# Performance work log

Hardware: AMD Instinct MI355X
Metric: run time of the kernel (lower is better)

## Reference

```python
import jax, jax.numpy as jnp
import numpy as np

EMBED_DIM = 1024
NUM_HEADS = 16
HEAD_DIM = EMBED_DIM // NUM_HEADS
BATCH = 2
SEQ = 2048


def setup_inputs() -> dict:
    key = jax.random.key(0)
    ks = jax.random.split(key, 9)
    scale = 1.0 / np.sqrt(EMBED_DIM)
    return {
        "inputs": jax.random.normal(ks[0], (BATCH, SEQ, EMBED_DIM), jnp.float32),
        "Wq": jax.random.normal(ks[1], (EMBED_DIM, EMBED_DIM), jnp.float32) * scale,
        "bq": jnp.zeros((EMBED_DIM,), jnp.float32),
        "Wk": jax.random.normal(ks[2], (EMBED_DIM, EMBED_DIM), jnp.float32) * scale,
        "bk": jnp.zeros((EMBED_DIM,), jnp.float32),
        "Wv": jax.random.normal(ks[3], (EMBED_DIM, EMBED_DIM), jnp.float32) * scale,
        "bv": jnp.zeros((EMBED_DIM,), jnp.float32),
        "Wo": jax.random.normal(ks[4], (EMBED_DIM, EMBED_DIM), jnp.float32) * scale,
        "bo": jnp.zeros((EMBED_DIM,), jnp.float32),
    }


def reference(inputs, Wq, bq, Wk, bk, Wv, bv, Wo, bo):
    B, S, D = inputs.shape
    H, Dh = NUM_HEADS, HEAD_DIM

    def split_heads(x):  # [B,S,D] -> [B,H,S,Dh]
        return x.reshape(B, S, H, Dh).transpose(0, 2, 1, 3)

    Q = split_heads(inputs @ Wq + bq)
    K = split_heads(inputs @ Wk + bk)
    V = split_heads(inputs @ Wv + bv)

    # naive full-score attention, faithful to the original
    scores = jnp.einsum("bhqd,bhkd->bhqk", Q, K) / jnp.sqrt(jnp.float32(Dh))
    weights = jax.nn.softmax(scores, axis=-1)
    out = jnp.einsum("bhqk,bhkd->bhqd", weights, V)

    concat = out.transpose(0, 2, 1, 3).reshape(B, S, D)
    return concat @ Wo + bo
```

## Files before the change

kernel.cpp:

```cpp
#include <hip/hip_runtime.h>

#define EMBED 1024
#define NHEAD 16
#define HDIM  64
#define BATCH 2
#define SEQ   2048
#define MTOK  (BATCH * SEQ)

typedef __bf16 bf16x8 __attribute__((ext_vector_type(8)));
typedef __bf16 bf16x4 __attribute__((ext_vector_type(4)));
typedef float  f32x4  __attribute__((ext_vector_type(4)));

__device__ __forceinline__ unsigned short f2bf(float f) {
  unsigned int u = __float_as_uint(f);
  u += 0x7fffu + ((u >> 16) & 1u);
  return (unsigned short)(u >> 16);
}
__device__ __forceinline__ __bf16 f2bf16(float f) {
  unsigned short s = f2bf(f);
  return *reinterpret_cast<__bf16*>(&s);
}

__device__ __forceinline__ void gload_lds16(const unsigned short* g, unsigned short* l) {
  __builtin_amdgcn_global_load_lds((__attribute__((address_space(1))) void*)g,
                                   (__attribute__((address_space(3))) void*)l, 16, 0, 0);
}

__global__ void cast_bf16_k(const float* __restrict__ src,
                            unsigned short* __restrict__ dst, int n4) {
  int i = blockIdx.x * blockDim.x + threadIdx.x;
  if (i < n4) {
    float4 f = reinterpret_cast<const float4*>(src)[i];
    ushort4 u;
    u.x = f2bf(f.x); u.y = f2bf(f.y); u.z = f2bf(f.z); u.w = f2bf(f.w);
    reinterpret_cast<ushort4*>(dst)[i] = u;
  }
}

__global__ __launch_bounds__(256)
void transpose_cast4_k(const float* __restrict__ s0, const float* __restrict__ s1,
                       const float* __restrict__ s2, const float* __restrict__ s3,
                       unsigned short* __restrict__ d0, unsigned short* __restrict__ d1,
                       unsigned short* __restrict__ d2, unsigned short* __restrict__ d3) {
  const float* s; unsigned short* d;
  switch (blockIdx.z) {
    case 0: s = s0; d = d0; break;
    case 1: s = s1; d = d1; break;
    case 2: s = s2; d = d2; break;
    default: s = s3; d = d3; break;
  }
  __shared__ unsigned short T[64][65];
  const int k0 = blockIdx.x * 64, n0 = blockIdx.y * 64;
  for (int i = threadIdx.x; i < 4096; i += 256) {
    int r = i >> 6, c = i & 63;
    T[c][r] = f2bf(s[(size_t)(k0 + r) * EMBED + n0 + c]);
  }
  __syncthreads();
  for (int i = threadIdx.x; i < 4096; i += 256) {
    int r = i >> 6, c = i & 63;
    d[(size_t)(n0 + r) * EMBED + k0 + c] = T[r][c];
  }
}

template<int MODE, int BM>
__global__ __launch_bounds__(256, 2)
void gemm_k(const unsigned short* __restrict__ A,
            const unsigned short* __restrict__ Bt,
            const float* __restrict__ b0, const float* __restrict__ b1,
            const float* __restrict__ b2,
            unsigned short* __restrict__ oQ, unsigned short* __restrict__ oK,
            unsigned short* __restrict__ oV, float* __restrict__ oF) {
  constexpr int MI = BM / 32;
  __shared__ unsigned short As[BM][64];
  __shared__ unsigned short Bs[128][64];
  const int tid = threadIdx.x, lane = tid & 63, wave = tid >> 6;
  const int lr = lane & 15, quad = lane >> 4;
  const int wm = (wave >> 1) * (BM / 2), wn = (wave & 1) * 64;
  const int row0 = blockIdx.x * BM, col0 = blockIdx.y * 128;
  const int srow = lane >> 3, sc = lane & 7;
  const int sw0 = (quad ^ (lr & 7)) * 8;
  const int sw1 = ((quad ^ 4) ^ (lr & 7)) * 8;

  const f32x4 fz = {0.f, 0.f, 0.f, 0.f};
  f32x4 acc[MI][4];
#pragma unroll
  for (int i = 0; i < MI; ++i)
#pragma unroll
    for (int j = 0; j < 4; ++j) acc[i][j] = fz;

  for (int k0 = 0; k0 < EMBED; k0 += 64) {
#pragma unroll
    for (int g = 0; g < BM / 32; ++g) {
      int rbase = wave * (BM / 4) + g * 8;
      int row = rbase + srow;
      gload_lds16(&A[(size_t)(row0 + row) * EMBED + k0 + ((sc ^ (row & 7)) * 8)],
                  &As[rbase][0]);
    }
#pragma unroll
    for (int g = 0; g < 4; ++g) {
      int rbase = wave * 32 + g * 8;
      int row = rbase + srow;
      gload_lds16(&Bt[(size_t)(col0 + row) * EMBED + k0 + ((sc ^ (row & 7)) * 8)],
                  &Bs[rbase][0]);
    }
    __syncthreads();
#pragma unroll
    for (int kk = 0; kk < 64; kk += 32) {
      const int so = (kk == 0) ? sw0 : sw1;
      bf16x8 af[MI], bv[4];
#pragma unroll
      for (int i = 0; i < MI; ++i)
        af[i] = *reinterpret_cast<const bf16x8*>(&As[wm + i * 16 + lr][so]);
#pragma unroll
      for (int j = 0; j < 4; ++j)
        bv[j] = *reinterpret_cast<const bf16x8*>(&Bs[wn + j * 16 + lr][so]);
#pragma unroll
      for (int i = 0; i < MI; ++i)
#pragma unroll
        for (int j = 0; j < 4; ++j)
          acc[i][j] = __builtin_amdgcn_mfma_f32_16x16x32_bf16(af[i], bv[j],
                                                              acc[i][j], 0, 0, 0);
    }
    __syncthreads();
  }

#pragma unroll
  for (int i = 0; i < MI; ++i) {
#pragma unroll
    for (int j = 0; j < 4; ++j) {
      const int col = col0 + wn + j * 16 + lr;
      if (MODE == 1) {
        const float bb = b0[col];
#pragma unroll
        for (int r = 0; r < 4; ++r) {
          const int row = row0 + wm + i * 16 + quad * 4 + r;
          oF[((size_t)row << 10) + col] = acc[i][j][r] + bb;
        }
      } else {
        const int which = col >> 10, cn = col & 1023;
        const float bb = (which == 0 ? b0 : which == 1 ? b1 : b2)[cn];
        const int h = cn >> 6, dd = cn & 63;
#pragma unroll
        for (int r = 0; r < 4; ++r) {
          const int row = row0 + wm + i * 16 + quad * 4 + r;
          const int b = row >> 11, ss = row & (SEQ - 1);
          float v = acc[i][j][r] + bb;
          if (which == 0) {
            oQ[((((size_t)b * NHEAD + h) * SEQ + ss) << 6) + dd] = f2bf(v * 0.125f);
          } else if (which == 1) {
            oK[((((size_t)b * NHEAD + h) * SEQ + ss) << 6) + dd] = f2bf(v);
          } else {
            oV[(((size_t)b * NHEAD + h) * HDIM + dd) * SEQ + ss] = f2bf(v);
          }
        }
      }
    }
  }
}

__global__ __launch_bounds__(256, 4)
void attn_k(const unsigned short* __restrict__ Qb,
            const unsigned short* __restrict__ Kb,
            const unsigned short* __restrict__ Vt,
            unsigned short* __restrict__ Ctx) {
  __shared__ unsigned short Qs[64][64];
  __shared__ unsigned short Ks[64][64];
  __shared__ unsigned short Vs[64][64];
  __shared__ unsigned short Ps[64][64];
  const int tid = threadIdx.x, lane = tid & 63, wave = tid >> 6;
  const int lr = lane & 15, quad = lane >> 4;
  const int qt = blockIdx.x, bh = blockIdx.y;
  const size_t base = (size_t)bh * SEQ * HDIM;
  const int srow = lane >> 3, sc = lane & 7;
  const int sw0 = (quad ^ (lr & 7)) * 8;
  const int sw1 = ((quad ^ 4) ^ (lr & 7)) * 8;

#pragma unroll
  for (int g = 0; g < 2; ++g) {
    int rbase = wave * 16 + g * 8;
    int row = rbase + srow;
    gload_lds16(&Qb[base + (size_t)(qt * 64 + row) * HDIM + ((sc ^ (row & 7)) * 8)],
                &Qs[rbase][0]);
  }
#pragma unroll
  for (int g = 0; g < 2; ++g) {
    int rbase = wave * 16 + g * 8;
    int row = rbase + srow;
    gload_lds16(&Kb[base + (size_t)row * HDIM + ((sc ^ (row & 7)) * 8)], &Ks[rbase][0]);
    gload_lds16(&Vt[base + (size_t)row * SEQ + ((sc ^ (row & 7)) * 8)], &Vs[rbase][0]);
  }
  __syncthreads();

  const bf16x8 qf0 = *reinterpret_cast<const bf16x8*>(&Qs[wave * 16 + lr][sw0]);
  const bf16x8 qf1 = *reinterpret_cast<const bf16x8*>(&Qs[wave * 16 + lr][sw1]);

  float m_run = -1e30f, l_run = 0.f;
  const f32x4 fz = {0.f, 0.f, 0.f, 0.f};
  f32x4 oacc[4];
#pragma unroll
  for (int d = 0; d < 4; ++d) oacc[d] = fz;

  for (int kt = 0;;) {
    f32x4 sc4[4];
#pragma unroll
    for (int nt = 0; nt < 4; ++nt) {
      bf16x8 kf0 = *reinterpret_cast<const bf16x8*>(&Ks[nt * 16 + lr][sw0]);
      bf16x8 kf1 = *reinterpret_cast<const bf16x8*>(&Ks[nt * 16 + lr][sw1]);
      f32x4 a = __builtin_amdgcn_mfma_f32_16x16x32_bf16(kf0, qf0, fz, 0, 0, 0);
      sc4[nt] = __builtin_amdgcn_mfma_f32_16x16x32_bf16(kf1, qf1, a, 0, 0, 0);
    }

    float mloc = -1e30f;
#pragma unroll
    for (int nt = 0; nt < 4; ++nt)
#pragma unroll
      for (int r = 0; r < 4; ++r) mloc = fmaxf(mloc, sc4[nt][r]);
    mloc = fmaxf(mloc, __shfl_xor(mloc, 16));
    mloc = fmaxf(mloc, __shfl_xor(mloc, 32));
    const float mnew = fmaxf(m_run, mloc);
    const float alpha = __expf(m_run - mnew);
    m_run = mnew;

    float psum = 0.f;
#pragma unroll
    for (int nt = 0; nt < 4; ++nt) {
      bf16x4 pk;
#pragma unroll
      for (int r = 0; r < 4; ++r) {
        float p = __expf(sc4[nt][r] - mnew);
        psum += p;
        pk[r] = f2bf16(p);
      }
      const int lc = nt * 2 + (quad >> 1);
      const int pc = lc ^ (lr & 7);
      *reinterpret_cast<bf16x4*>(&Ps[wave * 16 + lr][pc * 8 + (quad & 1) * 4]) = pk;
    }
    psum += __shfl_xor(psum, 16);
    psum += __shfl_xor(psum, 32);
    l_run = l_run * alpha + psum;

    float alr[4];
#pragma unroll
    for (int r = 0; r < 4; ++r) alr[r] = __shfl(alpha, quad * 4 + r);
#pragma unroll
    for (int d = 0; d < 4; ++d)
#pragma unroll
      for (int r = 0; r < 4; ++r) oacc[d][r] *= alr[r];

    __threadfence_block();

    const bf16x8 pa0 = *reinterpret_cast<const bf16x8*>(&Ps[wave * 16 + lr][sw0]);
    const bf16x8 pa1 = *reinterpret_cast<const bf16x8*>(&Ps[wave * 16 + lr][sw1]);
#pragma unroll
    for (int d = 0; d < 4; ++d) {
      bf16x8 vb0 = *reinterpret_cast<const bf16x8*>(&Vs[d * 16 + lr][sw0]);
      bf16x8 vb1 = *reinterpret_cast<const bf16x8*>(&Vs[d * 16 + lr][sw1]);
      oacc[d] = __builtin_amdgcn_mfma_f32_16x16x32_bf16(pa0, vb0, oacc[d], 0, 0, 0);
      oacc[d] = __builtin_amdgcn_mfma_f32_16x16x32_bf16(pa1, vb1, oacc[d], 0, 0, 0);
    }

    if (++kt == SEQ / 64) break;
    __syncthreads();
#pragma unroll
    for (int g = 0; g < 2; ++g) {
      int rbase = wave * 16 + g * 8;
      int row = rbase + srow;
      gload_lds16(&Kb[base + (size_t)(kt * 64 + row) * HDIM + ((sc ^ (row & 7)) * 8)],
                  &Ks[rbase][0]);
      gload_lds16(&Vt[base + (size_t)row * SEQ + kt * 64 + ((sc ^ (row & 7)) * 8)],
                  &Vs[rbase][0]);
    }
    __syncthreads();
  }

  const int b = bh >> 4, h = bh & 15;
  float linv[4];
#pragma unroll
  for (int r = 0; r < 4; ++r) linv[r] = 1.0f / __shfl(l_run, quad * 4 + r);
#pragma unroll
  for (int d = 0; d < 4; ++d)
#pragma unroll
    for (int r = 0; r < 4; ++r) {
      const int q = qt * 64 + wave * 16 + quad * 4 + r;
      Ctx[(((size_t)b * SEQ + q) << 10) + h * 64 + d * 16 + lr] =
          f2bf(oacc[d][r] * linv[r]);
    }
}

extern "C" void kernel_launch(void* const* d_in, const int* in_sizes, int n_in,
                              void* d_out, int out_size, void* d_ws, size_t ws_size,
                              hipStream_t stream) {
  const float* X  = (const float*)d_in[0];
  const float* Wq = (const float*)d_in[1];
  const float* bq = (const float*)d_in[2];
  const float* Wk = (const float*)d_in[3];
  const float* bk = (const float*)d_in[4];
  const float* Wv = (const float*)d_in[5];
  const float* bv = (const float*)d_in[6];
  const float* Wo = (const float*)d_in[7];
  const float* bo = (const float*)d_in[8];

  unsigned short* ws = (unsigned short*)d_ws;
  unsigned short* Xbf = ws;
  unsigned short* WqT = Xbf + (size_t)MTOK * EMBED;
  unsigned short* WkT = WqT + (size_t)EMBED * EMBED;
  unsigned short* WvT = WkT + (size_t)EMBED * EMBED;
  unsigned short* WoT = WvT + (size_t)EMBED * EMBED;
  unsigned short* Qb  = WoT + (size_t)EMBED * EMBED;
  unsigned short* Kb  = Qb + (size_t)MTOK * EMBED;
  unsigned short* Vt  = Kb + (size_t)MTOK * EMBED;
  unsigned short* Ctx = Vt + (size_t)MTOK * EMBED;

  cast_bf16_k<<<(MTOK * EMBED / 4 + 255) / 256, 256, 0, stream>>>(X, Xbf,
                                                                  MTOK * EMBED / 4);
  transpose_cast4_k<<<dim3(16, 16, 4), 256, 0, stream>>>(Wq, Wk, Wv, Wo,
                                                         WqT, WkT, WvT, WoT);

  gemm_k<0, 128><<<dim3(MTOK / 128, 3072 / 128), 256, 0, stream>>>(
      Xbf, WqT, bq, bk, bv, Qb, Kb, Vt, nullptr);

  attn_k<<<dim3(SEQ / 64, BATCH * NHEAD), 256, 0, stream>>>(Qb, Kb, Vt, Ctx);

  gemm_k<1, 64><<<dim3(MTOK / 64, EMBED / 128), 256, 0, stream>>>(
      Ctx, WoT, bo, nullptr, nullptr, nullptr, nullptr, nullptr, (float*)d_out);
}
```

Measured before the change: 210.7 us.

## Double-buffer K/V tiles in attention, use exp2 softmax, separate V transpose

Attention now double-buffers K and V tiles in LDS, prefetching the next tile while computing the current one, and drops one barrier per iteration. Softmax switches to exp2 with log2e folded into the Q scale. The QKV GEMM writes V row-major and a new transpose kernel produces V^T, replacing the strided scattered stores in the epilogue. Float-to-bf16 conversion moves from round-to-nearest-even to a cheaper round-half-up with packed perm. Occupancy hints and workspace buffer reuse also change. This adds an extra kernel launch and a V round trip through memory, and the rounding change slightly alters numerics.

```diff
diff --git a/kernel.cpp b/kernel.cpp
--- a/kernel.cpp
+++ b/kernel.cpp
@@ -6,19 +6,18 @@
 #define BATCH 2
 #define SEQ   2048
 #define MTOK  (BATCH * SEQ)
+#define QSCALE 0.1803368801f
 
 typedef __bf16 bf16x8 __attribute__((ext_vector_type(8)));
-typedef __bf16 bf16x4 __attribute__((ext_vector_type(4)));
 typedef float  f32x4  __attribute__((ext_vector_type(4)));
 
 __device__ __forceinline__ unsigned short f2bf(float f) {
-  unsigned int u = __float_as_uint(f);
-  u += 0x7fffu + ((u >> 16) & 1u);
-  return (unsigned short)(u >> 16);
-}
-__device__ __forceinline__ __bf16 f2bf16(float f) {
-  unsigned short s = f2bf(f);
-  return *reinterpret_cast<__bf16*>(&s);
+  return (unsigned short)((__float_as_uint(f) + 0x8000u) >> 16);
+}
+__device__ __forceinline__ unsigned int pkbf(float a, float b) {
+  unsigned int ua = __float_as_uint(a) + 0x8000u;
+  unsigned int ub = __float_as_uint(b) + 0x8000u;
+  return __builtin_amdgcn_perm(ub, ua, 0x07060302u);
 }
 
 __device__ __forceinline__ void gload_lds16(const unsigned short* g, unsigned short* l) {
@@ -31,9 +30,8 @@
   int i = blockIdx.x * blockDim.x + threadIdx.x;
   if (i < n4) {
     float4 f = reinterpret_cast<const float4*>(src)[i];
-    ushort4 u;
-    u.x = f2bf(f.x); u.y = f2bf(f.y); u.z = f2bf(f.z); u.w = f2bf(f.w);
-    reinterpret_cast<ushort4*>(dst)[i] = u;
+    uint2 u = make_uint2(pkbf(f.x, f.y), pkbf(f.z, f.w));
+    reinterpret_cast<uint2*>(dst)[i] = u;
   }
 }
 
@@ -62,8 +60,28 @@
   }
 }
 
+__global__ __launch_bounds__(256)
+void vtrans_k(const unsigned short* __restrict__ Vn,
+              unsigned short* __restrict__ Vt) {
+  __shared__ unsigned short T[64][65];
+  const int s0 = blockIdx.x * 64;
+  const size_t base = (size_t)blockIdx.y * SEQ * HDIM;
+  for (int i = threadIdx.x; i < 1024; i += 256) {
+    int r = i >> 4, c4 = (i & 15) * 4;
+    ushort4 v = *reinterpret_cast<const ushort4*>(&Vn[base + (size_t)(s0 + r) * HDIM + c4]);
+    T[c4][r] = v.x; T[c4 + 1][r] = v.y; T[c4 + 2][r] = v.z; T[c4 + 3][r] = v.w;
+  }
+  __syncthreads();
+  for (int i = threadIdx.x; i < 1024; i += 256) {
+    int r = i >> 4, c4 = (i & 15) * 4;
+    ushort4 v;
+    v.x = T[r][c4]; v.y = T[r][c4 + 1]; v.z = T[r][c4 + 2]; v.w = T[r][c4 + 3];
+    *reinterpret_cast<ushort4*>(&Vt[base + (size_t)r * SEQ + s0 + c4]) = v;
+  }
+}
+
 template<int MODE, int BM>
-__global__ __launch_bounds__(256, 2)
+__global__ __launch_bounds__(256, MODE == 0 ? 3 : 4)
 void gemm_k(const unsigned short* __restrict__ A,
             const unsigned short* __restrict__ Bt,
             const float* __restrict__ b0, const float* __restrict__ b1,
@@ -139,33 +157,29 @@
       } else {
         const int which = col >> 10, cn = col & 1023;
         const float bb = (which == 0 ? b0 : which == 1 ? b1 : b2)[cn];
+        unsigned short* o = (which == 0 ? oQ : which == 1 ? oK : oV);
+        const float sscale = (which == 0) ? QSCALE : 1.0f;
         const int h = cn >> 6, dd = cn & 63;
 #pragma unroll
         for (int r = 0; r < 4; ++r) {
           const int row = row0 + wm + i * 16 + quad * 4 + r;
           const int b = row >> 11, ss = row & (SEQ - 1);
-          float v = acc[i][j][r] + bb;
-          if (which == 0) {
-            oQ[((((size_t)b * NHEAD + h) * SEQ + ss) << 6) + dd] = f2bf(v * 0.125f);
-          } else if (which == 1) {
-            oK[((((size_t)b * NHEAD + h) * SEQ + ss) << 6) + dd] = f2bf(v);
-          } else {
-            oV[(((size_t)b * NHEAD + h) * HDIM + dd) * SEQ + ss] = f2bf(v);
-          }
+          o[((((size_t)b * NHEAD + h) * SEQ + ss) << 6) + dd] =
+              f2bf((acc[i][j][r] + bb) * sscale);
         }
       }
     }
   }
 }
 
-__global__ __launch_bounds__(256, 4)
+__global__ __launch_bounds__(256, 3)
 void attn_k(const unsigned short* __restrict__ Qb,
             const unsigned short* __restrict__ Kb,
             const unsigned short* __restrict__ Vt,
             unsigned short* __restrict__ Ctx) {
   __shared__ unsigned short Qs[64][64];
-  __shared__ unsigned short Ks[64][64];
-  __shared__ unsigned short Vs[64][64];
+  __shared__ unsigned short Ks[2][64][64];
+  __shared__ unsigned short Vs[2][64][64];
   __shared__ unsigned short Ps[64][64];
   const int tid = threadIdx.x, lane = tid & 63, wave = tid >> 6;
   const int lr = lane & 15, quad = lane >> 4;
@@ -181,13 +195,10 @@
     int row = rbase + srow;
     gload_lds16(&Qb[base + (size_t)(qt * 64 + row) * HDIM + ((sc ^ (row & 7)) * 8)],
                 &Qs[rbase][0]);
-  }
-#pragma unroll
-  for (int g = 0; g < 2; ++g) {
-    int rbase = wave * 16 + g * 8;
-    int row = rbase + srow;
-    gload_lds16(&Kb[base + (size_t)row * HDIM + ((sc ^ (row & 7)) * 8)], &Ks[rbase][0]);
-    gload_lds16(&Vt[base + (size_t)row * SEQ + ((sc ^ (row & 7)) * 8)], &Vs[rbase][0]);
+    gload_lds16(&Kb[base + (size_t)row * HDIM + ((sc ^ (row & 7)) * 8)],
+                &Ks[0][rbase][0]);
+    gload_lds16(&Vt[base + (size_t)row * SEQ + ((sc ^ (row & 7)) * 8)],
+                &Vs[0][rbase][0]);
   }
   __syncthreads();
 
@@ -196,44 +207,53 @@
 
   float m_run = -1e30f, l_run = 0.f;
   const f32x4 fz = {0.f, 0.f, 0.f, 0.f};
-  f32x4 oacc[4];
-#pragma unroll
-  for (int d = 0; d < 4; ++d) oacc[d] = fz;
-
-  for (int kt = 0;;) {
+  f32x4 oacc[4] = {fz, fz, fz, fz};
+
+  for (int kt = 0; kt < SEQ / 64; ++kt) {
+    const int buf = kt & 1;
+    if (kt + 1 < SEQ / 64) {
+#pragma unroll
+      for (int g = 0; g < 2; ++g) {
+        int rbase = wave * 16 + g * 8;
+        int row = rbase + srow;
+        gload_lds16(&Kb[base + (size_t)((kt + 1) * 64 + row) * HDIM + ((sc ^ (row & 7)) * 8)],
+                    &Ks[buf ^ 1][rbase][0]);
+        gload_lds16(&Vt[base + (size_t)row * SEQ + (kt + 1) * 64 + ((sc ^ (row & 7)) * 8)],
+                    &Vs[buf ^ 1][rbase][0]);
+      }
+    }
+
     f32x4 sc4[4];
 #pragma unroll
     for (int nt = 0; nt < 4; ++nt) {
-      bf16x8 kf0 = *reinterpret_cast<const bf16x8*>(&Ks[nt * 16 + lr][sw0]);
-      bf16x8 kf1 = *reinterpret_cast<const bf16x8*>(&Ks[nt * 16 + lr][sw1]);
+      bf16x8 kf0 = *reinterpret_cast<const bf16x8*>(&Ks[buf][nt * 16 + lr][sw0]);
+      bf16x8 kf1 = *reinterpret_cast<const bf16x8*>(&Ks[buf][nt * 16 + lr][sw1]);
       f32x4 a = __builtin_amdgcn_mfma_f32_16x16x32_bf16(kf0, qf0, fz, 0, 0, 0);
       sc4[nt] = __builtin_amdgcn_mfma_f32_16x16x32_bf16(kf1, qf1, a, 0, 0, 0);
     }
 
-    float mloc = -1e30f;
-#pragma unroll
-    for (int nt = 0; nt < 4; ++nt)
-#pragma unroll
-      for (int r = 0; r < 4; ++r) mloc = fmaxf(mloc, sc4[nt][r]);
+    float mloc = fmaxf(fmaxf(fmaxf(sc4[0][0], sc4[0][1]), fmaxf(sc4[0][2], sc4[0][3])),
+                       fmaxf(fmaxf(sc4[1][0], sc4[1][1]), fmaxf(sc4[1][2], sc4[1][3])));
+    mloc = fmaxf(mloc,
+                 fmaxf(fmaxf(fmaxf(sc4[2][0], sc4[2][1]), fmaxf(sc4[2][2], sc4[2][3])),
+                       fmaxf(fmaxf(sc4[3][0], sc4[3][1]), fmaxf(sc4[3][2], sc4[3][3]))));
     mloc = fmaxf(mloc, __shfl_xor(mloc, 16));
     mloc = fmaxf(mloc, __shfl_xor(mloc, 32));
     const float mnew = fmaxf(m_run, mloc);
-    const float alpha = __expf(m_run - mnew);
+    const float alpha = __builtin_amdgcn_exp2f(m_run - mnew);
     m_run = mnew;
 
     float psum = 0.f;
 #pragma unroll
     for (int nt = 0; nt < 4; ++nt) {
-      bf16x4 pk;
-#pragma unroll
-      for (int r = 0; r < 4; ++r) {
-        float p = __expf(sc4[nt][r] - mnew);
-        psum += p;
-        pk[r] = f2bf16(p);
-      }
-      const int lc = nt * 2 + (quad >> 1);
-      const int pc = lc ^ (lr & 7);
-      *reinterpret_cast<bf16x4*>(&Ps[wave * 16 + lr][pc * 8 + (quad & 1) * 4]) = pk;
+      float p0 = __builtin_amdgcn_exp2f(sc4[nt][0] - mnew);
+      float p1 = __builtin_amdgcn_exp2f(sc4[nt][1] - mnew);
+      float p2 = __builtin_amdgcn_exp2f(sc4[nt][2] - mnew);
+      float p3 = __builtin_amdgcn_exp2f(sc4[nt][3] - mnew);
+      psum += (p0 + p1) + (p2 + p3);
+      const int pc = (nt * 2 + (quad >> 1)) ^ (lr & 7);
+      *reinterpret_cast<uint2*>(&Ps[wave * 16 + lr][pc * 8 + (quad & 1) * 4]) =
+          make_uint2(pkbf(p0, p1), pkbf(p2, p3));
     }
     psum += __shfl_xor(psum, 16);
     psum += __shfl_xor(psum, 32);
@@ -253,24 +273,14 @@
     const bf16x8 pa1 = *reinterpret_cast<const bf16x8*>(&Ps[wave * 16 + lr][sw1]);
 #pragma unroll
     for (int d = 0; d < 4; ++d) {
-      bf16x8 vb0 = *reinterpret_cast<const bf16x8*>(&Vs[d * 16 + lr][sw0]);
-      bf16x8 vb1 = *reinterpret_cast<const bf16x8*>(&Vs[d * 16 + lr][sw1]);
+      bf16x8 vb0 = *reinterpret_cast<const bf16x8*>(&Vs[buf][d * 16 + lr][sw0]);
+      bf16x8 vb1 = *reinterpret_cast<const bf16x8*>(&Vs[buf][d * 16 + lr][sw1]);
       oacc[d] = __builtin_amdgcn_mfma_f32_16x16x32_bf16(pa0, vb0, oacc[d], 0, 0, 0);
       oacc[d] = __builtin_amdgcn_mfma_f32_16x16x32_bf16(pa1, vb1, oacc[d], 0, 0, 0);
     }
 
-    if (++kt == SEQ / 64) break;
-    __syncthreads();
-#pragma unroll
-    for (int g = 0; g < 2; ++g) {
-      int rbase = wave * 16 + g * 8;
-      int row = rbase + srow;
-      gload_lds16(&Kb[base + (size_t)(kt * 64 + row) * HDIM + ((sc ^ (row & 7)) * 8)],
-                  &Ks[rbase][0]);
-      gload_lds16(&Vt[base + (size_t)row * SEQ + kt * 64 + ((sc ^ (row & 7)) * 8)],
-                  &Vs[rbase][0]);
-    }
-    __syncthreads();
+    if (kt + 1 < SEQ / 64)
+      __syncthreads();
   }
 
   const int b = bh >> 4, h = bh & 15;
@@ -301,23 +311,26 @@
   const float* bo = (const float*)d_in[8];
 
   unsigned short* ws = (unsigned short*)d_ws;
+  const size_t M1 = (size_t)1024 * 1024;
   unsigned short* Xbf = ws;
-  unsigned short* WqT = Xbf + (size_t)MTOK * EMBED;
-  unsigned short* WkT = WqT + (size_t)EMBED * EMBED;
-  unsigned short* WvT = WkT + (size_t)EMBED * EMBED;
-  unsigned short* WoT = WvT + (size_t)EMBED * EMBED;
-  unsigned short* Qb  = WoT + (size_t)EMBED * EMBED;
-  unsigned short* Kb  = Qb + (size_t)MTOK * EMBED;
-  unsigned short* Vt  = Kb + (size_t)MTOK * EMBED;
-  unsigned short* Ctx = Vt + (size_t)MTOK * EMBED;
-
-  cast_bf16_k<<<(MTOK * EMBED / 4 + 255) / 256, 256, 0, stream>>>(X, Xbf,
-                                                                  MTOK * EMBED / 4);
+  unsigned short* WqT = ws + 4 * M1;
+  unsigned short* WkT = ws + 5 * M1;
+  unsigned short* WvT = ws + 6 * M1;
+  unsigned short* WoT = ws + 7 * M1;
+  unsigned short* Qb  = ws + 8 * M1;
+  unsigned short* Kb  = ws + 12 * M1;
+  unsigned short* Vn  = ws + 16 * M1;
+  unsigned short* Vt  = Xbf;
+  unsigned short* Ctx = Vn;
+
+  cast_bf16_k<<<4096, 256, 0, stream>>>(X, Xbf, MTOK * EMBED / 4);
   transpose_cast4_k<<<dim3(16, 16, 4), 256, 0, stream>>>(Wq, Wk, Wv, Wo,
                                                          WqT, WkT, WvT, WoT);
 
   gemm_k<0, 128><<<dim3(MTOK / 128, 3072 / 128), 256, 0, stream>>>(
-      Xbf, WqT, bq, bk, bv, Qb, Kb, Vt, nullptr);
+      Xbf, WqT, bq, bk, bv, Qb, Kb, Vn, nullptr);
+
+  vtrans_k<<<dim3(SEQ / 64, BATCH * NHEAD), 256, 0, stream>>>(Vn, Vt);
 
   attn_k<<<dim3(SEQ / 64, BATCH * NHEAD), 256, 0, stream>>>(Qb, Kb, Vt, Ctx);
 
```

New measurement: 232.3 us. 10.2% more time.
